# Optimization experiments

Measured on AMD Instinct MI355X. Metric: run time of the kernel, lower is better.

## Reference

```python
import jax, jax.numpy as jnp
import numpy as np
jax.config.update("jax_enable_x64", True)

SR = 44100
STATE_SIZE = 4096
RG0, R10, C10, C20 = 1.0e6, 4.7e5, 3.3e-9, 1.0e-9

# Reconstructed DK-method incidence matrices (3 circuit nodes, 1 vsrc):
#   Vin at node1; C1 node1->node2; R1 node2->gnd; pot top node2->node3;
#   pot bottom node3->gnd; C2 node3->gnd; output at node3 (pot wiper).
_Nu = np.array([[1., 0., 0.]])
_Nx = np.array([[1., -1., 0.], [0., 0., 1.]])
_Nr = np.array([[0., 1., 0.]])
_Nv = np.array([[0., 1., -1.], [0., 0., 1.]])
_No = np.array([[0., 0., 1.]])


def _preamp_forward(x, cond, state, alpha_rg, alpha_r1, alpha_c1, alpha_c2, cond_w, cond_b):
    f64 = jnp.float64
    T = 1.0 / SR
    Nu, Nx, Nr, Nv, No = (jnp.asarray(m, f64) for m in (_Nu, _Nx, _Nr, _Nv, _No))
    Zm = jnp.eye(2, dtype=f64)
    n_nodes, n_vsrc = 3, 1
    zpad = jnp.zeros((2, n_vsrc), f64)
    Nvp = jnp.concatenate([Nv, zpad], axis=1)                      # [2,4]
    Nxp = jnp.concatenate([Nx, zpad], axis=1)                      # [2,4]
    Nop = jnp.concatenate([No, jnp.zeros((1, n_vsrc), f64)], 1)    # [1,4]
    Nup = jnp.concatenate([jnp.zeros((n_nodes, n_vsrc), f64), jnp.eye(n_vsrc, dtype=f64)], 0)  # [4,1]

    # component updates (sigmoid-trimmed around nominal values)
    RG = (0.9 + jax.nn.sigmoid(alpha_rg[0]).astype(f64) * 0.2) * RG0
    R1 = (0.99 + jax.nn.sigmoid(alpha_r1[0]).astype(f64) * 0.02) * R10
    C1 = (0.9 + jax.nn.sigmoid(alpha_c1[0]).astype(f64) * 0.2) * C10
    C2 = (0.9 + jax.nn.sigmoid(alpha_c2[0]).astype(f64) * 0.2) * C20
    Gr = jnp.reshape(1.0 / R1, (1, 1))
    Gx = jnp.diag(jnp.stack([2.0 * C1 / T, 2.0 * C2 / T]))

    # cond block: affine -> sigmoid -> log pot taper
    pot = jax.nn.sigmoid(cond[:, 0] * cond_w[0] + cond_b[0])
    p = jnp.clip((jnp.power(10.0, pot) - 1.0) / 9.0, 1e-4, 1.0 - 1e-4).astype(f64)  # [B]

    # state-space update
    top = jnp.concatenate([Nr.T @ Gr @ Nr + Nx.T @ Gx @ Nx, Nu.T], axis=1)
    bot = jnp.concatenate([Nu, jnp.zeros((n_vsrc, n_vsrc), f64)], axis=1)
    So_inv = jnp.linalg.inv(jnp.concatenate([top, bot], axis=0))   # [4,4]
    Q = Nvp @ So_inv @ Nvp.T                                        # [2,2]
    Ux = Nxp @ So_inv @ Nvp.T                                       # [2,2]
    Uo = Nop @ So_inv @ Nvp.T                                       # [1,2]
    Uu = Nup.T @ So_inv @ Nvp.T                                     # [1,2]
    ZGx = 2.0 * Zm @ Gx
    Ao = ZGx @ Nxp @ So_inv @ Nxp.T - Zm
    Bo = ZGx @ Nxp @ So_inv @ Nup
    Do = Nop @ So_inv @ Nxp.T
    Eo = Nop @ So_inv @ Nup

    d = jnp.stack([(1.0 - p) * RG, p * RG], axis=-1)                # [B,2]
    Rv = d[:, :, None] * jnp.eye(2, dtype=f64)                      # [B,2,2] diag
    RvQ = jnp.linalg.inv(Rv + Q)                                    # [B,2,2]

    ZGxUx = ZGx @ Ux
    A = Ao - ZGxUx @ RvQ @ Ux.T                                     # [B,2,2]
    Bm = Bo - ZGxUx @ RvQ @ Uu.T                                    # [B,2,1]
    Dm = Do - Uo @ RvQ @ Ux.T                                       # [B,1,2]
    Em = Eo - Uo @ RvQ @ Uu.T                                       # [B,1,1]

    # quadratic characteristic poly [1, -tr, det] (= real part of prod(z-eig))
    def poly2(M):
        tr = M[..., 0, 0] + M[..., 1, 1]
        det = M[..., 0, 0] * M[..., 1, 1] - M[..., 0, 1] * M[..., 1, 0]
        return jnp.stack([jnp.ones_like(tr), -tr, det], axis=-1)    # [B,3]

    den = poly2(A)
    num = poly2(A - Bm @ Dm) + (Em[:, 0] - 1.0) * den

    nb = 1 + STATE_SIZE // 2
    z = jnp.exp(-1j * jnp.linspace(0.0, jnp.pi, nb))                # complex128 [nb]

    def polyval(c):  # Horner, highest degree first
        c = c.astype(jnp.complex128)
        return (c[:, 0, None] * z + c[:, 1, None]) * z + c[:, 2, None]  # [B,nb]

    h = polyval(num) / polyval(den)                                 # [B,nb]

    L = x.shape[1]
    st = jnp.concatenate([state[:, L:, :], x], axis=1).astype(f64)  # [B,S,1]
    sf = jnp.fft.rfft(st, axis=1)                                   # [B,nb,1]
    out = jnp.fft.irfft(sf * h[:, :, None], axis=1).astype(jnp.float32)
    return out[:, -L:, :]


def setup_inputs() -> dict:
    key = jax.random.key(0)
    k0, k1, k2 = jax.random.split(key, 3)
    B, L = 2048, 2048
    return {
        "x": jax.random.normal(k0, (B, L, 1), dtype=jnp.float32),
        "cond": jax.random.uniform(k1, (B, 1), dtype=jnp.float32),
        "state": jax.random.normal(k2, (B, STATE_SIZE, 1), dtype=jnp.float32) * 0.1,
        "alpha_rg": jnp.zeros((1,), jnp.float32),
        "alpha_r1": jnp.zeros((1,), jnp.float32),
        "alpha_c1": jnp.zeros((1,), jnp.float32),
        "alpha_c2": jnp.zeros((1,), jnp.float32),
        "cond_w": jnp.ones((1,), jnp.float32),
        "cond_b": jnp.zeros((1,), jnp.float32),
    }


def reference(x, cond, state, alpha_rg, alpha_r1, alpha_c1, alpha_c2, cond_w, cond_b):
    return _preamp_forward(x, cond, state, alpha_rg, alpha_r1, alpha_c1, alpha_c2, cond_w, cond_b)
```

## Files before the change

### kernel.cpp

```cpp
#include <hip/hip_runtime.h>
#include <math.h>

#define NFFT 4096
#define LSEG 2048
#define SSZ 4096

typedef float v4f __attribute__((ext_vector_type(4)));

__global__ __launch_bounds__(256, 4)
void preamp_iir_kernel(const float* __restrict__ x,
                       const float* __restrict__ state,
                       const float* __restrict__ cond,
                       const float* __restrict__ a_rg,
                       const float* __restrict__ a_r1,
                       const float* __restrict__ a_c1,
                       const float* __restrict__ a_c2,
                       const float* __restrict__ cond_w,
                       const float* __restrict__ cond_b,
                       float* __restrict__ out, int B) {
    __shared__ float cf[13];
    __shared__ float Tw[2][4];

    const int t = threadIdx.x;
    const int b = blockIdx.x;
    const int lane = t & 63;
    const int wv = t >> 6;

    const float* xb  = x + (size_t)b * LSEG;
    const float* stb = state + (size_t)b * SSZ + (SSZ - LSEG);

    float s[16];
    if (t < 128) {
#pragma unroll
        for (int u = 0; u < 4; ++u) {
            const int g0 = 4092 - 16 * t - 4 * u;
            v4f v = *(const v4f*)(xb + (g0 - LSEG));
            s[4 * u + 0] = v.w; s[4 * u + 1] = v.z;
            s[4 * u + 2] = v.y; s[4 * u + 3] = v.x;
        }
    } else {
#pragma unroll
        for (int u = 0; u < 4; ++u) {
            const int g0 = 4092 - 16 * t - 4 * u;
            v4f v = *(const v4f*)(stb + g0);
            s[4 * u + 0] = v.w; s[4 * u + 1] = v.z;
            s[4 * u + 2] = v.y; s[4 * u + 3] = v.x;
        }
    }

    if (t == 0) {
        const double RG = (0.9 + (double)(1.0f / (1.0f + expf(-a_rg[0]))) * 0.2) * 1.0e6;
        const double R1 = (0.99 + (double)(1.0f / (1.0f + expf(-a_r1[0]))) * 0.02) * 4.7e5;
        const double C1 = (0.9 + (double)(1.0f / (1.0f + expf(-a_c1[0]))) * 0.2) * 3.3e-9;
        const double C2 = (0.9 + (double)(1.0f / (1.0f + expf(-a_c2[0]))) * 0.2) * 1.0e-9;
        const double g1 = 1.0 / R1;
        const double gc1 = 2.0 * C1 * 44100.0;
        const double gc2 = 2.0 * C2 * 44100.0;

        float zf = cond[b] * cond_w[0] + cond_b[0];
        float pot = 1.0f / (1.0f + expf(-zf));
        float prf = (powf(10.0f, pot) - 1.0f) / 9.0f;
        prf = fminf(fmaxf(prf, 1e-4f), 1.0f - 1e-4f);
        const double p = (double)prf;

        const double ds = gc1 + g1;
        double S[4][4] = {
            {0.0, 0.0,        0.0,       1.0},
            {0.0, 1.0 / ds,   0.0,       gc1 / ds},
            {0.0, 0.0,        1.0 / gc2, 0.0},
            {1.0, gc1 / ds,   0.0,       -gc1 * g1 / ds}};

        double Q00 = S[1][1] - S[1][2] - S[2][1] + S[2][2];
        double Q01 = S[1][2] - S[2][2];
        double Q10 = S[2][1] - S[2][2];
        double Q11 = S[2][2];

        double Ux00 = S[0][1] - S[0][2] - S[1][1] + S[1][2];
        double Ux01 = S[0][2] - S[1][2];
        double Ux10 = S[2][1] - S[2][2];
        double Ux11 = S[2][2];

        double Uo0 = S[2][1] - S[2][2], Uo1 = S[2][2];
        double Uu0 = S[3][1] - S[3][2], Uu1 = S[3][2];

        double P00 = S[0][0] - S[0][1] - S[1][0] + S[1][1];
        double P01 = S[0][2] - S[1][2];
        double P10 = S[2][0] - S[2][1];
        double P11 = S[2][2];

        double Ao00 = 2.0 * gc1 * P00 - 1.0, Ao01 = 2.0 * gc1 * P01;
        double Ao10 = 2.0 * gc2 * P10,       Ao11 = 2.0 * gc2 * P11 - 1.0;

        double Bo0 = 2.0 * gc1 * (S[0][3] - S[1][3]);
        double Bo1 = 2.0 * gc2 * S[2][3];

        double Do0 = S[2][0] - S[2][1], Do1 = S[2][2];
        double Eo  = S[2][3];

        double T00 = 2.0 * gc1 * Ux00, T01 = 2.0 * gc1 * Ux01;
        double T10 = 2.0 * gc2 * Ux10, T11 = 2.0 * gc2 * Ux11;

        double d0 = (1.0 - p) * RG, d1v = p * RG;
        double M00 = d0 + Q00, M01 = Q01, M10 = Q10, M11 = d1v + Q11;
        double idet = 1.0 / (M00 * M11 - M01 * M10);
        double G00 =  M11 * idet, G01 = -M01 * idet;
        double G10 = -M10 * idet, G11 =  M00 * idet;

        double TG00 = T00 * G00 + T01 * G10, TG01 = T00 * G01 + T01 * G11;
        double TG10 = T10 * G00 + T11 * G10, TG11 = T10 * G01 + T11 * G11;

        double A00 = Ao00 - (TG00 * Ux00 + TG01 * Ux01);
        double A01 = Ao01 - (TG00 * Ux10 + TG01 * Ux11);
        double A10 = Ao10 - (TG10 * Ux00 + TG11 * Ux01);
        double A11 = Ao11 - (TG10 * Ux10 + TG11 * Ux11);

        double Bm0 = Bo0 - (TG00 * Uu0 + TG01 * Uu1);
        double Bm1 = Bo1 - (TG10 * Uu0 + TG11 * Uu1);

        double w0v = Uo0 * G00 + Uo1 * G10, w1v = Uo0 * G01 + Uo1 * G11;
        double Dm0 = Do0 - (w0v * Ux00 + w1v * Ux01);
        double Dm1 = Do1 - (w0v * Ux10 + w1v * Ux11);
        double Em  = Eo  - (w0v * Uu0 + w1v * Uu1);

        double den1 = -(A00 + A11);
        double den2 = A00 * A11 - A01 * A10;
        double Mm00 = A00 - Bm0 * Dm0, Mm01 = A01 - Bm0 * Dm1;
        double Mm10 = A10 - Bm1 * Dm0, Mm11 = A11 - Bm1 * Dm1;
        double num0 = Em;
        double num1 = -(Mm00 + Mm11) + (Em - 1.0) * den1;
        double num2 = (Mm00 * Mm11 - Mm01 * Mm10) + (Em - 1.0) * den2;

        double trA  = A00 + A11;
        double disc = den1 * den1 - 4.0 * den2;
        double sq   = sqrt(disc > 0.0 ? disc : 0.0);
        double L1d  = 0.5 * (trA + sq);
        double L2d  = 0.5 * (trA - sq);
        double nv1 = (num0 * L1d + num1) * L1d + num2;
        double nv2 = (num0 * L2d + num1) * L2d + num2;
        double C0d =  num2 / den2;
        double C1d =  nv1 / (L1d * sq);
        double C2d = -nv2 / (L2d * sq);
        double a2 = L1d * L1d, a4 = a2 * a2, a8 = a4 * a4, F16a = a8 * a8;
        double a32 = F16a * F16a, a64 = a32 * a32, a128 = a64 * a64,
               a256 = a128 * a128, a512 = a256 * a256, F1ka = a512 * a512;
        double F4ka = (F1ka * F1ka) * (F1ka * F1ka);
        double b2 = L2d * L2d, b4 = b2 * b2, b8 = b4 * b4, F16b = b8 * b8;
        double b32 = F16b * F16b, b64 = b32 * b32, b128 = b64 * b64,
               b256 = b128 * b128, b512 = b256 * b256, F1kb = b512 * b512;
        double F4kb = (F1kb * F1kb) * (F1kb * F1kb);

        cf[0]  = (float)L1d;
        cf[1]  = (float)L2d;
        cf[2]  = (float)C0d;
        cf[3]  = (float)C1d;
        cf[4]  = (float)C2d;
        cf[5]  = (float)F16a;
        cf[6]  = (float)F16b;
        cf[7]  = 16.0f * log2f((float)L1d);
        cf[8]  = 16.0f * log2f((float)L2d);
        cf[9]  = (float)F1ka;
        cf[10] = (float)F1kb;
        cf[11] = (float)(1.0 / (1.0 - F4ka));
        cf[12] = (float)(1.0 / (1.0 - F4kb));
    }
    __syncthreads();

    const float lam1 = cf[0], lam2 = cf[1];
    const float c0 = cf[2], c1 = cf[3], c2 = cf[4];
    const float f16a = cf[5], f16b = cf[6];
    const float l2a = cf[7], l2b = cf[8];
    const float f1ka = cf[9], f1kb = cf[10];
    const float ioma = cf[11], iomb = cf[12];

    float w1 = 0.0f, w2 = 0.0f;
#pragma unroll
    for (int j = 0; j < 16; ++j) {
        w1 = fmaf(lam1, w1, s[j]);
        w2 = fmaf(lam2, w2, s[j]);
    }

    float f1 = f16a, f2 = f16b;
#pragma unroll
    for (int d = 1; d < 64; d <<= 1) {
        float o1 = __shfl_up(w1, d);
        float o2 = __shfl_up(w2, d);
        if (lane >= d) { w1 = fmaf(f1, o1, w1); w2 = fmaf(f2, o2, w2); }
        f1 *= f1; f2 *= f2;
    }
    if (lane == 63) { Tw[0][wv] = w1; Tw[1][wv] = w2; }
    __syncthreads();

    if (t < 128) {
        float S1 = 0.0f, S2 = 0.0f;
        if (wv == 1) { S1 = Tw[0][0]; S2 = Tw[1][0]; }
        const float el1 = exp2f((float)lane * l2a);
        const float el2 = exp2f((float)lane * l2b);
        w1 = fmaf(el1 * f16a, S1, w1);
        w2 = fmaf(el2 * f16b, S2, w2);
        float p1 = __shfl_up(w1, 1); if (lane == 0) p1 = S1;
        float p2 = __shfl_up(w2, 1); if (lane == 0) p2 = S2;

        float K1 = fmaf(fmaf(fmaf(Tw[0][0], f1ka, Tw[0][1]), f1ka, Tw[0][2]), f1ka, Tw[0][3]) * ioma;
        float K2 = fmaf(fmaf(fmaf(Tw[1][0], f1kb, Tw[1][1]), f1kb, Tw[1][2]), f1kb, Tw[1][3]) * iomb;

        const float pw1 = el1 * (wv ? f1ka : 1.0f);
        const float pw2 = el2 * (wv ? f1kb : 1.0f);
        float w1r = fmaf(pw1, K1, p1);
        float w2r = fmaf(pw2, K2, p2);

        float* ob = out + (size_t)b * LSEG;
#pragma unroll
        for (int u = 0; u < 4; ++u) {
            float y0, y1, y2, y3;
            {
                const float sv = s[4 * u + 0];
                w1r = fmaf(lam1, w1r, sv); w2r = fmaf(lam2, w2r, sv);
                y0 = fmaf(c0, sv, fmaf(c2, w2r, c1 * w1r));
            }
            {
                const float sv = s[4 * u + 1];
                w1r = fmaf(lam1, w1r, sv); w2r = fmaf(lam2, w2r, sv);
                y1 = fmaf(c0, sv, fmaf(c2, w2r, c1 * w1r));
            }
            {
                const float sv = s[4 * u + 2];
                w1r = fmaf(lam1, w1r, sv); w2r = fmaf(lam2, w2r, sv);
                y2 = fmaf(c0, sv, fmaf(c2, w2r, c1 * w1r));
            }
            {
                const float sv = s[4 * u + 3];
                w1r = fmaf(lam1, w1r, sv); w2r = fmaf(lam2, w2r, sv);
                y3 = fmaf(c0, sv, fmaf(c2, w2r, c1 * w1r));
            }
            v4f o;
            o.x = y3; o.y = y2; o.z = y1; o.w = y0;
            *(v4f*)(ob + (2044 - 16 * t - 4 * u)) = o;
        }
    }
}

extern "C" void kernel_launch(void* const* d_in, const int* in_sizes, int n_in,
                              void* d_out, int out_size, void* d_ws, size_t ws_size,
                              hipStream_t stream) {
    const float* x     = (const float*)d_in[0];
    const float* cond  = (const float*)d_in[1];
    const float* state = (const float*)d_in[2];
    const float* a_rg  = (const float*)d_in[3];
    const float* a_r1  = (const float*)d_in[4];
    const float* a_c1  = (const float*)d_in[5];
    const float* a_c2  = (const float*)d_in[6];
    const float* c_w   = (const float*)d_in[7];
    const float* c_b   = (const float*)d_in[8];
    float* out = (float*)d_out;

    const int B = in_sizes[1];

    preamp_iir_kernel<<<dim3(B), dim3(256), 0, stream>>>(
        x, state, cond, a_rg, a_r1, a_c1, a_c2, c_w, c_b, out, B);
}
```

Before: 104.5 us.

## Process two batch rows per block with packed float2 recurrence

Each block now handles two batch rows instead of one. Their samples are packed into float2 vectors so the recurrence, the wave scan and the output stage run on both rows together, which may map to packed FP32 instructions. Two threads compute the per-row coefficients in parallel. This halves the grid and amortizes the serial double-precision coefficient setup and the barriers across two rows, at the cost of more registers per thread and fewer blocks in flight.

```diff
diff --git a/kernel.cpp b/kernel.cpp
--- a/kernel.cpp
+++ b/kernel.cpp
@@ -5,7 +5,12 @@
 #define LSEG 2048
 #define SSZ 4096
 
+typedef float v2f __attribute__((ext_vector_type(2)));
 typedef float v4f __attribute__((ext_vector_type(4)));
+
+static __device__ __forceinline__ v2f vfma(v2f a, v2f b, v2f c) {
+    return (v2f){fmaf(a.x, b.x, c.x), fmaf(a.y, b.y, c.y)};
+}
 
 __global__ __launch_bounds__(256, 4)
 void preamp_iir_kernel(const float* __restrict__ x,
@@ -18,37 +23,45 @@
                        const float* __restrict__ cond_w,
                        const float* __restrict__ cond_b,
                        float* __restrict__ out, int B) {
-    __shared__ float cf[13];
-    __shared__ float Tw[2][4];
+    __shared__ float cf[26];
+    __shared__ v2f Tw[2][4];
 
     const int t = threadIdx.x;
-    const int b = blockIdx.x;
+    const int b0 = 2 * blockIdx.x;
+    const int b1 = (b0 + 1 < B) ? b0 + 1 : b0;
     const int lane = t & 63;
     const int wv = t >> 6;
 
-    const float* xb  = x + (size_t)b * LSEG;
-    const float* stb = state + (size_t)b * SSZ + (SSZ - LSEG);
-
-    float s[16];
+    const float* xa  = x + (size_t)b0 * LSEG;
+    const float* sta = state + (size_t)b0 * SSZ + (SSZ - LSEG);
+    const float* xbp = x + (size_t)b1 * LSEG;
+    const float* stb = state + (size_t)b1 * SSZ + (SSZ - LSEG);
+
+    v2f s[16];
     if (t < 128) {
 #pragma unroll
         for (int u = 0; u < 4; ++u) {
             const int g0 = 4092 - 16 * t - 4 * u;
-            v4f v = *(const v4f*)(xb + (g0 - LSEG));
-            s[4 * u + 0] = v.w; s[4 * u + 1] = v.z;
-            s[4 * u + 2] = v.y; s[4 * u + 3] = v.x;
+            v4f va = *(const v4f*)(xa + (g0 - LSEG));
+            v4f vb = *(const v4f*)(xbp + (g0 - LSEG));
+            s[4 * u + 0] = (v2f){va.w, vb.w}; s[4 * u + 1] = (v2f){va.z, vb.z};
+            s[4 * u + 2] = (v2f){va.y, vb.y}; s[4 * u + 3] = (v2f){va.x, vb.x};
         }
     } else {
 #pragma unroll
         for (int u = 0; u < 4; ++u) {
             const int g0 = 4092 - 16 * t - 4 * u;
-            v4f v = *(const v4f*)(stb + g0);
-            s[4 * u + 0] = v.w; s[4 * u + 1] = v.z;
-            s[4 * u + 2] = v.y; s[4 * u + 3] = v.x;
+            v4f va = *(const v4f*)(sta + g0);
+            v4f vb = *(const v4f*)(stb + g0);
+            s[4 * u + 0] = (v2f){va.w, vb.w}; s[4 * u + 1] = (v2f){va.z, vb.z};
+            s[4 * u + 2] = (v2f){va.y, vb.y}; s[4 * u + 3] = (v2f){va.x, vb.x};
         }
     }
 
-    if (t == 0) {
+    if ((t & 127) == 0) {
+        const int who = t >> 7;
+        const int bb = who ? b1 : b0;
+
         const double RG = (0.9 + (double)(1.0f / (1.0f + expf(-a_rg[0]))) * 0.2) * 1.0e6;
         const double R1 = (0.99 + (double)(1.0f / (1.0f + expf(-a_r1[0]))) * 0.02) * 4.7e5;
         const double C1 = (0.9 + (double)(1.0f / (1.0f + expf(-a_c1[0]))) * 0.2) * 3.3e-9;
@@ -57,7 +70,7 @@
         const double gc1 = 2.0 * C1 * 44100.0;
         const double gc2 = 2.0 * C2 * 44100.0;
 
-        float zf = cond[b] * cond_w[0] + cond_b[0];
+        float zf = cond[bb] * cond_w[0] + cond_b[0];
         float pot = 1.0f / (1.0f + expf(-zf));
         float prf = (powf(10.0f, pot) - 1.0f) / 9.0f;
         prf = fminf(fmaxf(prf, 1e-4f), 1.0f - 1e-4f);
@@ -149,92 +162,100 @@
                b256 = b128 * b128, b512 = b256 * b256, F1kb = b512 * b512;
         double F4kb = (F1kb * F1kb) * (F1kb * F1kb);
 
-        cf[0]  = (float)L1d;
-        cf[1]  = (float)L2d;
-        cf[2]  = (float)C0d;
-        cf[3]  = (float)C1d;
-        cf[4]  = (float)C2d;
-        cf[5]  = (float)F16a;
-        cf[6]  = (float)F16b;
-        cf[7]  = 16.0f * log2f((float)L1d);
-        cf[8]  = 16.0f * log2f((float)L2d);
-        cf[9]  = (float)F1ka;
-        cf[10] = (float)F1kb;
-        cf[11] = (float)(1.0 / (1.0 - F4ka));
-        cf[12] = (float)(1.0 / (1.0 - F4kb));
+        cf[0  + who] = (float)L1d;
+        cf[2  + who] = (float)L2d;
+        cf[4  + who] = (float)C0d;
+        cf[6  + who] = (float)C1d;
+        cf[8  + who] = (float)C2d;
+        cf[10 + who] = (float)F16a;
+        cf[12 + who] = (float)F16b;
+        cf[14 + who] = 16.0f * log2f((float)L1d);
+        cf[16 + who] = 16.0f * log2f((float)L2d);
+        cf[18 + who] = (float)F1ka;
+        cf[20 + who] = (float)F1kb;
+        cf[22 + who] = (float)(1.0 / (1.0 - F4ka));
+        cf[24 + who] = (float)(1.0 / (1.0 - F4kb));
     }
     __syncthreads();
 
-    const float lam1 = cf[0], lam2 = cf[1];
-    const float c0 = cf[2], c1 = cf[3], c2 = cf[4];
-    const float f16a = cf[5], f16b = cf[6];
-    const float l2a = cf[7], l2b = cf[8];
-    const float f1ka = cf[9], f1kb = cf[10];
-    const float ioma = cf[11], iomb = cf[12];
-
-    float w1 = 0.0f, w2 = 0.0f;
+    const v2f lam1 = {cf[0],  cf[1]},  lam2 = {cf[2],  cf[3]};
+    const v2f c0   = {cf[4],  cf[5]},  c1   = {cf[6],  cf[7]},  c2 = {cf[8], cf[9]};
+    const v2f f16a = {cf[10], cf[11]}, f16b = {cf[12], cf[13]};
+    const v2f l2a  = {cf[14], cf[15]}, l2b  = {cf[16], cf[17]};
+    const v2f f1ka = {cf[18], cf[19]}, f1kb = {cf[20], cf[21]};
+    const v2f ioma = {cf[22], cf[23]}, iomb = {cf[24], cf[25]};
+
+    v2f w1 = {0.0f, 0.0f}, w2 = {0.0f, 0.0f};
 #pragma unroll
     for (int j = 0; j < 16; ++j) {
-        w1 = fmaf(lam1, w1, s[j]);
-        w2 = fmaf(lam2, w2, s[j]);
-    }
-
-    float f1 = f16a, f2 = f16b;
+        w1 = vfma(lam1, w1, s[j]);
+        w2 = vfma(lam2, w2, s[j]);
+    }
+
+    v2f f1 = f16a, f2 = f16b;
 #pragma unroll
     for (int d = 1; d < 64; d <<= 1) {
-        float o1 = __shfl_up(w1, d);
-        float o2 = __shfl_up(w2, d);
-        if (lane >= d) { w1 = fmaf(f1, o1, w1); w2 = fmaf(f2, o2, w2); }
-        f1 *= f1; f2 *= f2;
+        v2f o1 = {__shfl_up(w1.x, d), __shfl_up(w1.y, d)};
+        v2f o2 = {__shfl_up(w2.x, d), __shfl_up(w2.y, d)};
+        if (lane >= d) { w1 = vfma(f1, o1, w1); w2 = vfma(f2, o2, w2); }
+        f1 = (v2f){f1.x * f1.x, f1.y * f1.y};
+        f2 = (v2f){f2.x * f2.x, f2.y * f2.y};
     }
     if (lane == 63) { Tw[0][wv] = w1; Tw[1][wv] = w2; }
     __syncthreads();
 
     if (t < 128) {
-        float S1 = 0.0f, S2 = 0.0f;
+        v2f S1 = {0.0f, 0.0f}, S2 = {0.0f, 0.0f};
         if (wv == 1) { S1 = Tw[0][0]; S2 = Tw[1][0]; }
-        const float el1 = exp2f((float)lane * l2a);
-        const float el2 = exp2f((float)lane * l2b);
-        w1 = fmaf(el1 * f16a, S1, w1);
-        w2 = fmaf(el2 * f16b, S2, w2);
-        float p1 = __shfl_up(w1, 1); if (lane == 0) p1 = S1;
-        float p2 = __shfl_up(w2, 1); if (lane == 0) p2 = S2;
-
-        float K1 = fmaf(fmaf(fmaf(Tw[0][0], f1ka, Tw[0][1]), f1ka, Tw[0][2]), f1ka, Tw[0][3]) * ioma;
-        float K2 = fmaf(fmaf(fmaf(Tw[1][0], f1kb, Tw[1][1]), f1kb, Tw[1][2]), f1kb, Tw[1][3]) * iomb;
-
-        const float pw1 = el1 * (wv ? f1ka : 1.0f);
-        const float pw2 = el2 * (wv ? f1kb : 1.0f);
-        float w1r = fmaf(pw1, K1, p1);
-        float w2r = fmaf(pw2, K2, p2);
-
-        float* ob = out + (size_t)b * LSEG;
+        const v2f el1 = {exp2f((float)lane * l2a.x), exp2f((float)lane * l2a.y)};
+        const v2f el2 = {exp2f((float)lane * l2b.x), exp2f((float)lane * l2b.y)};
+        w1 = vfma((v2f){el1.x * f16a.x, el1.y * f16a.y}, S1, w1);
+        w2 = vfma((v2f){el2.x * f16b.x, el2.y * f16b.y}, S2, w2);
+        v2f p1 = {__shfl_up(w1.x, 1), __shfl_up(w1.y, 1)};
+        v2f p2 = {__shfl_up(w2.x, 1), __shfl_up(w2.y, 1)};
+        if (lane == 0) { p1 = S1; p2 = S2; }
+
+        v2f K1 = vfma(vfma(vfma(Tw[0][0], f1ka, Tw[0][1]), f1ka, Tw[0][2]), f1ka, Tw[0][3]);
+        v2f K2 = vfma(vfma(vfma(Tw[1][0], f1kb, Tw[1][1]), f1kb, Tw[1][2]), f1kb, Tw[1][3]);
+        K1 = (v2f){K1.x * ioma.x, K1.y * ioma.y};
+        K2 = (v2f){K2.x * iomb.x, K2.y * iomb.y};
+
+        const v2f one = {1.0f, 1.0f};
+        const v2f pf1 = wv ? f1ka : one;
+        const v2f pf2 = wv ? f1kb : one;
+        v2f w1r = vfma((v2f){el1.x * pf1.x, el1.y * pf1.y}, K1, p1);
+        v2f w2r = vfma((v2f){el2.x * pf2.x, el2.y * pf2.y}, K2, p2);
+
+        float* oa = out + (size_t)b0 * LSEG;
+        float* ob = out + (size_t)b1 * LSEG;
 #pragma unroll
         for (int u = 0; u < 4; ++u) {
-            float y0, y1, y2, y3;
-            {
-                const float sv = s[4 * u + 0];
-                w1r = fmaf(lam1, w1r, sv); w2r = fmaf(lam2, w2r, sv);
-                y0 = fmaf(c0, sv, fmaf(c2, w2r, c1 * w1r));
-            }
-            {
-                const float sv = s[4 * u + 1];
-                w1r = fmaf(lam1, w1r, sv); w2r = fmaf(lam2, w2r, sv);
-                y1 = fmaf(c0, sv, fmaf(c2, w2r, c1 * w1r));
-            }
-            {
-                const float sv = s[4 * u + 2];
-                w1r = fmaf(lam1, w1r, sv); w2r = fmaf(lam2, w2r, sv);
-                y2 = fmaf(c0, sv, fmaf(c2, w2r, c1 * w1r));
-            }
-            {
-                const float sv = s[4 * u + 3];
-                w1r = fmaf(lam1, w1r, sv); w2r = fmaf(lam2, w2r, sv);
-                y3 = fmaf(c0, sv, fmaf(c2, w2r, c1 * w1r));
-            }
-            v4f o;
-            o.x = y3; o.y = y2; o.z = y1; o.w = y0;
-            *(v4f*)(ob + (2044 - 16 * t - 4 * u)) = o;
+            v2f y0, y1, y2, y3;
+            {
+                const v2f sv = s[4 * u + 0];
+                w1r = vfma(lam1, w1r, sv); w2r = vfma(lam2, w2r, sv);
+                y0 = vfma(c0, sv, vfma(c2, w2r, (v2f){c1.x * w1r.x, c1.y * w1r.y}));
+            }
+            {
+                const v2f sv = s[4 * u + 1];
+                w1r = vfma(lam1, w1r, sv); w2r = vfma(lam2, w2r, sv);
+                y1 = vfma(c0, sv, vfma(c2, w2r, (v2f){c1.x * w1r.x, c1.y * w1r.y}));
+            }
+            {
+                const v2f sv = s[4 * u + 2];
+                w1r = vfma(lam1, w1r, sv); w2r = vfma(lam2, w2r, sv);
+                y2 = vfma(c0, sv, vfma(c2, w2r, (v2f){c1.x * w1r.x, c1.y * w1r.y}));
+            }
+            {
+                const v2f sv = s[4 * u + 3];
+                w1r = vfma(lam1, w1r, sv); w2r = vfma(lam2, w2r, sv);
+                y3 = vfma(c0, sv, vfma(c2, w2r, (v2f){c1.x * w1r.x, c1.y * w1r.y}));
+            }
+            const int o0 = 2044 - 16 * t - 4 * u;
+            v4f oA; oA.x = y3.x; oA.y = y2.x; oA.z = y1.x; oA.w = y0.x;
+            *(v4f*)(oa + o0) = oA;
+            v4f oB; oB.x = y3.y; oB.y = y2.y; oB.z = y1.y; oB.w = y0.y;
+            *(v4f*)(ob + o0) = oB;
         }
     }
 }
@@ -255,6 +276,6 @@
 
     const int B = in_sizes[1];
 
-    preamp_iir_kernel<<<dim3(B), dim3(256), 0, stream>>>(
+    preamp_iir_kernel<<<dim3((B + 1) / 2), dim3(256), 0, stream>>>(
         x, state, cond, a_rg, a_r1, a_c1, a_c2, c_w, c_b, out, B);
 }
```

Result: no change. 105.7 us (+1.2%).
